# Kernel optimization log

Measured on AMD Instinct MI355X. Metric: run time of the kernel, lower is better.

Reference implementation:

```python
import jax, jax.numpy as jnp
import numpy as np

TEMPERATURE = 0.07
EPS = 1e-8  # torch CosineSimilarity eps default


def setup_inputs() -> dict:
    key = jax.random.key(0)
    k1, k2 = jax.random.split(key)
    N, D = 8192, 1024
    image_features = jax.random.normal(k1, (N, D), dtype=jnp.float32)
    text_features = jax.random.normal(k2, (N, D), dtype=jnp.float32)
    return {"image_features": image_features, "text_features": text_features}


def _normalize(x):
    # matches torch cosine similarity denominator clamp: norm >= eps
    n = jnp.sqrt(jnp.sum(x * x, axis=-1, keepdims=True))
    return x / jnp.maximum(n, EPS)


def reference(image_features, text_features):
    # cosine similarity via normalize + GEMM (same math as broadcasted NxNxD form)
    img_n = _normalize(image_features)  # [N, D]
    txt_n = _normalize(text_features)   # [N, D]
    logits = jnp.einsum('id,jd->ij', img_n, txt_n) / TEMPERATURE  # [N, N]

    N = logits.shape[0]
    labels = jnp.arange(N)
    # cross-entropy with labels = diagonal indices
    logp_i2t = jax.nn.log_softmax(logits, axis=-1)      # rows: image -> text
    logp_t2i = jax.nn.log_softmax(logits.T, axis=-1)    # rows: text -> image
    loss_i2t = -jnp.mean(logp_i2t[labels, labels])
    loss_t2i = -jnp.mean(logp_t2i[labels, labels])
    return (loss_i2t + loss_t2i) / 2
```

## Files before the change

kernel.cpp:

```cpp
#include <hip/hip_runtime.h>


#define BM 128
#define BN 128
#define BKB 128

typedef float floatx4 __attribute__((ext_vector_type(4)));
typedef int   intx4   __attribute__((ext_vector_type(4)));
typedef int   intx8   __attribute__((ext_vector_type(8)));

__device__ __forceinline__ void gload_lds16(const unsigned char* g, unsigned char* lds) {
    __builtin_amdgcn_global_load_lds(
        (const __attribute__((address_space(1))) void*)g,
        (__attribute__((address_space(3))) void*)lds,
        16, 0, 0);
}

__global__ __launch_bounds__(256)
void normalize_fp8(const float* __restrict__ img, const float* __restrict__ txt,
                   unsigned int* __restrict__ oimg, unsigned int* __restrict__ otxt,
                   float* __restrict__ sums, float* __restrict__ out, int N) {
    const int gi = blockIdx.x * 256 + threadIdx.x;
    if (gi < 2 * N) sums[gi] = 0.f;
    if (gi == 0) out[0] = 0.f;

    const int gw = blockIdx.x * 4 + (threadIdx.x >> 6);
    const int lane = threadIdx.x & 63;
    const float* in = (gw < N) ? img : txt;
    unsigned int* o = (gw < N) ? oimg : otxt;
    const int row = (gw < N) ? gw : gw - N;
    const float4* rp = (const float4*)(in + (size_t)row * 1024);

    float4 v[4];
    float ss = 0.f;
    #pragma unroll
    for (int j = 0; j < 4; ++j) {
        v[j] = rp[j * 64 + lane];
        ss += v[j].x * v[j].x + v[j].y * v[j].y + v[j].z * v[j].z + v[j].w * v[j].w;
    }
    #pragma unroll
    for (int o2 = 1; o2 < 64; o2 <<= 1) ss += __shfl_xor(ss, o2);
    const float inv = 16.0f / fmaxf(sqrtf(ss), 1e-8f);
    #pragma unroll
    for (int j = 0; j < 4; ++j) {
        int p = __builtin_amdgcn_cvt_pk_fp8_f32(v[j].x * inv, v[j].y * inv, 0, false);
        p = __builtin_amdgcn_cvt_pk_fp8_f32(v[j].z * inv, v[j].w * inv, p, true);
        o[(size_t)row * 256 + j * 64 + lane] = (unsigned int)p;
    }
}

__global__ __launch_bounds__(256)
void gemm_exp_kernel(const unsigned char* __restrict__ A,
                     const unsigned char* __restrict__ B,
                     float* __restrict__ rowsum, float* __restrict__ colsum,
                     float* __restrict__ diag, int K, float scale) {
    __shared__ unsigned char As[2 * BM * 64];
    __shared__ unsigned char Bs[2 * BN * 64];

    const int bm = blockIdx.x, bn = blockIdx.y;
    const int tid = threadIdx.x;
    const int lane = tid & 63;
    const int wave = tid >> 6;
    const int quad = lane >> 4;
    const int lanelo = lane & 15;
    const int wrow = (wave >> 1) * 64;
    const int wcol = (wave & 1) * 64;

    floatx4 acc[4][4] = {};

    const int c0 = wave * 128 + lane;
    const int c1 = c0 + 64;
    const int r0 = c0 >> 2, r1 = c1 >> 2;
    const int kg0 = ((c0 & 3) ^ ((r0 >> 1) & 3)) * 16;
    const int kg1 = ((c1 & 3) ^ ((r1 >> 1) & 3)) * 16;

    const unsigned char* pa0 = A + (size_t)bm * BM * K + (size_t)r0 * K + kg0;
    const unsigned char* pa1 = A + (size_t)bm * BM * K + (size_t)r1 * K + kg1;
    const unsigned char* pb0 = B + (size_t)bn * BN * K + (size_t)r0 * K + kg0;
    const unsigned char* pb1 = B + (size_t)bn * BN * K + (size_t)r1 * K + kg1;
    unsigned char* dA0 = As + c0 * 16;
    unsigned char* dA1 = As + c1 * 16;
    unsigned char* dB0 = Bs + c0 * 16;
    unsigned char* dB1 = Bs + c1 * 16;

    int aoff[4], boff[4];
    #pragma unroll
    for (int t = 0; t < 4; ++t) {
        const int Ra = wrow + t * 16 + lanelo;
        const int Rb = wcol + t * 16 + lanelo;
        const int cA = (quad & 1) * 2;
        aoff[t] = (quad >> 1) * 8192 + Ra * 64 + ((cA ^ ((Ra >> 1) & 3)) * 16);
        boff[t] = (quad >> 1) * 8192 + Rb * 64 + ((cA ^ ((Rb >> 1) & 3)) * 16);
    }

    for (int k0 = 0; k0 < K; k0 += BKB) {
        #pragma unroll
        for (int w = 0; w < 2; ++w) {
            gload_lds16(pa0 + w * 64, dA0 + w * 8192);
            gload_lds16(pa1 + w * 64, dA1 + w * 8192);
            gload_lds16(pb0 + w * 64, dB0 + w * 8192);
            gload_lds16(pb1 + w * 64, dB1 + w * 8192);
        }
        pa0 += BKB; pa1 += BKB; pb0 += BKB; pb1 += BKB;
        __syncthreads();

        intx8 af[4], bg[4];
        #pragma unroll
        for (int t = 0; t < 4; ++t) {
            const intx4 alo = *(const intx4*)(As + aoff[t]);
            const intx4 ahi = *(const intx4*)(As + (aoff[t] ^ 16));
            af[t] = __builtin_shufflevector(alo, ahi, 0, 1, 2, 3, 4, 5, 6, 7);
            const intx4 blo = *(const intx4*)(Bs + boff[t]);
            const intx4 bhi = *(const intx4*)(Bs + (boff[t] ^ 16));
            bg[t] = __builtin_shufflevector(blo, bhi, 0, 1, 2, 3, 4, 5, 6, 7);
        }

        #pragma unroll
        for (int tm = 0; tm < 4; ++tm)
            #pragma unroll
            for (int tn = 0; tn < 4; ++tn)
                acc[tm][tn] = __builtin_amdgcn_mfma_scale_f32_16x16x128_f8f6f4(
                    af[tm], bg[tn], acc[tm][tn],
                    0, 0,
                    0, 127,
                    0, 127);
        __syncthreads();
    }

    const int growb = bm * BM + wrow;
    const int gcolb = bn * BN + wcol;

    #pragma unroll
    for (int tm = 0; tm < 4; ++tm)
        #pragma unroll
        for (int tn = 0; tn < 4; ++tn)
            #pragma unroll
            for (int r = 0; r < 4; ++r) {
                const float l = acc[tm][tn][r] * scale;
                const int grow = growb + tm * 16 + quad * 4 + r;
                const int gcol = gcolb + tn * 16 + lanelo;
                if (grow == gcol) diag[grow] = l;
                acc[tm][tn][r] = __expf(l);
            }

    #pragma unroll
    for (int tm = 0; tm < 4; ++tm) {
        floatx4 rs = acc[tm][0] + acc[tm][1] + acc[tm][2] + acc[tm][3];
        #pragma unroll
        for (int r = 0; r < 4; ++r) {
            float v = rs[r];
            v += __shfl_xor(v, 1);
            v += __shfl_xor(v, 2);
            v += __shfl_xor(v, 4);
            v += __shfl_xor(v, 8);
            if (lanelo == 0)
                atomicAdd(&rowsum[growb + tm * 16 + quad * 4 + r], v);
        }
    }

    #pragma unroll
    for (int tn = 0; tn < 4; ++tn) {
        float cs = 0.f;
        #pragma unroll
        for (int tm = 0; tm < 4; ++tm)
            cs += acc[tm][tn][0] + acc[tm][tn][1] + acc[tm][tn][2] + acc[tm][tn][3];
        cs += __shfl_xor(cs, 16);
        cs += __shfl_xor(cs, 32);
        if (quad == 0)
            atomicAdd(&colsum[gcolb + tn * 16 + lanelo], cs);
    }
}

__global__ __launch_bounds__(256)
void final_reduce(const float* __restrict__ rowsum, const float* __restrict__ colsum,
                  const float* __restrict__ diag, float* __restrict__ out, int n) {
    const int i = blockIdx.x * 256 + threadIdx.x;
    const int t = threadIdx.x;
    float v = 0.5f * (logf(rowsum[i]) + logf(colsum[i])) - diag[i];
    #pragma unroll
    for (int o = 1; o < 64; o <<= 1) v += __shfl_xor(v, o);
    __shared__ float ws[4];
    if ((t & 63) == 0) ws[t >> 6] = v;
    __syncthreads();
    if (t == 0) atomicAdd(out, (ws[0] + ws[1] + ws[2] + ws[3]) / (float)n);
}

extern "C" void kernel_launch(void* const* d_in, const int* in_sizes, int n_in,
                              void* d_out, int out_size, void* d_ws, size_t ws_size,
                              hipStream_t stream) {
    const float* img = (const float*)d_in[0];
    const float* txt = (const float*)d_in[1];
    float* out = (float*)d_out;

    const int D = 1024;
    const int N = in_sizes[0] / D;

    unsigned char* imgq = (unsigned char*)d_ws;
    unsigned char* txtq = imgq + (size_t)N * D;
    float* rowsum = (float*)(txtq + (size_t)N * D);
    float* colsum = rowsum + N;
    float* diag = colsum + N;

    normalize_fp8<<<2 * N / 4, 256, 0, stream>>>(img, txt, (unsigned int*)imgq,
                                                 (unsigned int*)txtq, rowsum, out, N);

    dim3 grid(N / BM, N / BN);
    gemm_exp_kernel<<<grid, 256, 0, stream>>>(imgq, txtq, rowsum, colsum, diag,
                                              D, 1.0f / (256.0f * 0.07f));
    final_reduce<<<N / 256, 256, 0, stream>>>(rowsum, colsum, diag, out, N);
}
```

Measured before the change: 196.4 us.

## Load GEMM fragments directly from global memory instead of staging through LDS

The FP8 GEMM no longer stages A/B tiles in shared memory. Each lane now reads its MFMA operand fragments straight from global memory with 16-byte vector loads, which removes both block barriers and the LDS round trip. The cost is lost data sharing inside the block: each wave pair re-reads the same rows, so global and L2 traffic goes up. There is also no explicit prefetch, so load latency is hidden only by occupancy and compiler scheduling.

Result: slower. 327.3 us (+66.7%).

```diff
diff --git a/kernel.cpp b/kernel.cpp
--- a/kernel.cpp
+++ b/kernel.cpp
@@ -8,13 +8,6 @@
 typedef float floatx4 __attribute__((ext_vector_type(4)));
 typedef int   intx4   __attribute__((ext_vector_type(4)));
 typedef int   intx8   __attribute__((ext_vector_type(8)));
-
-__device__ __forceinline__ void gload_lds16(const unsigned char* g, unsigned char* lds) {
-    __builtin_amdgcn_global_load_lds(
-        (const __attribute__((address_space(1))) void*)g,
-        (__attribute__((address_space(3))) void*)lds,
-        16, 0, 0);
-}
 
 __global__ __launch_bounds__(256)
 void normalize_fp8(const float* __restrict__ img, const float* __restrict__ txt,
@@ -54,9 +47,6 @@
                      const unsigned char* __restrict__ B,
                      float* __restrict__ rowsum, float* __restrict__ colsum,
                      float* __restrict__ diag, int K, float scale) {
-    __shared__ unsigned char As[2 * BM * 64];
-    __shared__ unsigned char Bs[2 * BN * 64];
-
     const int bm = blockIdx.x, bn = blockIdx.y;
     const int tid = threadIdx.x;
     const int lane = tid & 63;
@@ -68,51 +58,30 @@
 
     floatx4 acc[4][4] = {};
 
-    const int c0 = wave * 128 + lane;
-    const int c1 = c0 + 64;
-    const int r0 = c0 >> 2, r1 = c1 >> 2;
-    const int kg0 = ((c0 & 3) ^ ((r0 >> 1) & 3)) * 16;
-    const int kg1 = ((c1 & 3) ^ ((r1 >> 1) & 3)) * 16;
-
-    const unsigned char* pa0 = A + (size_t)bm * BM * K + (size_t)r0 * K + kg0;
-    const unsigned char* pa1 = A + (size_t)bm * BM * K + (size_t)r1 * K + kg1;
-    const unsigned char* pb0 = B + (size_t)bn * BN * K + (size_t)r0 * K + kg0;
-    const unsigned char* pb1 = B + (size_t)bn * BN * K + (size_t)r1 * K + kg1;
-    unsigned char* dA0 = As + c0 * 16;
-    unsigned char* dA1 = As + c1 * 16;
-    unsigned char* dB0 = Bs + c0 * 16;
-    unsigned char* dB1 = Bs + c1 * 16;
-
-    int aoff[4], boff[4];
+    const unsigned char* pa[4];
+    const unsigned char* pb[4];
     #pragma unroll
     for (int t = 0; t < 4; ++t) {
-        const int Ra = wrow + t * 16 + lanelo;
-        const int Rb = wcol + t * 16 + lanelo;
-        const int cA = (quad & 1) * 2;
-        aoff[t] = (quad >> 1) * 8192 + Ra * 64 + ((cA ^ ((Ra >> 1) & 3)) * 16);
-        boff[t] = (quad >> 1) * 8192 + Rb * 64 + ((cA ^ ((Rb >> 1) & 3)) * 16);
+        pa[t] = A + (size_t)(bm * BM + wrow + t * 16 + lanelo) * K + quad * 32;
+        pb[t] = B + (size_t)(bn * BN + wcol + t * 16 + lanelo) * K + quad * 32;
     }
 
     for (int k0 = 0; k0 < K; k0 += BKB) {
+        intx4 a0[4], a1[4], b0[4], b1[4];
         #pragma unroll
-        for (int w = 0; w < 2; ++w) {
-            gload_lds16(pa0 + w * 64, dA0 + w * 8192);
-            gload_lds16(pa1 + w * 64, dA1 + w * 8192);
-            gload_lds16(pb0 + w * 64, dB0 + w * 8192);
-            gload_lds16(pb1 + w * 64, dB1 + w * 8192);
+        for (int t = 0; t < 4; ++t) {
+            a0[t] = *(const intx4*)(pa[t]);
+            a1[t] = *(const intx4*)(pa[t] + 16);
+            b0[t] = *(const intx4*)(pb[t]);
+            b1[t] = *(const intx4*)(pb[t] + 16);
+            pa[t] += BKB; pb[t] += BKB;
         }
-        pa0 += BKB; pa1 += BKB; pb0 += BKB; pb1 += BKB;
-        __syncthreads();
 
         intx8 af[4], bg[4];
         #pragma unroll
         for (int t = 0; t < 4; ++t) {
-            const intx4 alo = *(const intx4*)(As + aoff[t]);
-            const intx4 ahi = *(const intx4*)(As + (aoff[t] ^ 16));
-            af[t] = __builtin_shufflevector(alo, ahi, 0, 1, 2, 3, 4, 5, 6, 7);
-            const intx4 blo = *(const intx4*)(Bs + boff[t]);
-            const intx4 bhi = *(const intx4*)(Bs + (boff[t] ^ 16));
-            bg[t] = __builtin_shufflevector(blo, bhi, 0, 1, 2, 3, 4, 5, 6, 7);
+            af[t] = __builtin_shufflevector(a0[t], a1[t], 0, 1, 2, 3, 4, 5, 6, 7);
+            bg[t] = __builtin_shufflevector(b0[t], b1[t], 0, 1, 2, 3, 4, 5, 6, 7);
         }
 
         #pragma unroll
@@ -124,7 +93,6 @@
                     0, 0,
                     0, 127,
                     0, 127);
-        __syncthreads();
     }
 
     const int growb = bm * BM + wrow;
```

## Switch FP8 GEMM to 32x32x64 scaled MFMA tiles

Applied to the files above, without the earlier changes.

Replaces the 4x4 grid of 16x16x128 scaled FP8 MFMAs per wave with a 2x2 grid of 32x32x64 MFMAs, issued over two K sub-steps per 128-wide LDS tile. The LDS fragment offsets, the epilogue row/column index mapping, and the row/column sum shuffle reductions are rewritten for the 32x32 accumulator layout. The goal is fewer LDS fragment reads per MFMA and fewer instructions for the same FLOPs. It also adds a launch-bounds occupancy hint of 4 blocks, which may constrain register allocation.

Result: slower. 208.7 us (+6.3%).

```diff
diff --git a/kernel.cpp b/kernel.cpp
--- a/kernel.cpp
+++ b/kernel.cpp
@@ -5,9 +5,9 @@
 #define BN 128
 #define BKB 128
 
-typedef float floatx4 __attribute__((ext_vector_type(4)));
-typedef int   intx4   __attribute__((ext_vector_type(4)));
-typedef int   intx8   __attribute__((ext_vector_type(8)));
+typedef float floatx16 __attribute__((ext_vector_type(16)));
+typedef int   intx4    __attribute__((ext_vector_type(4)));
+typedef int   intx8    __attribute__((ext_vector_type(8)));
 
 __device__ __forceinline__ void gload_lds16(const unsigned char* g, unsigned char* lds) {
     __builtin_amdgcn_global_load_lds(
@@ -49,7 +49,7 @@
     }
 }
 
-__global__ __launch_bounds__(256)
+__global__ __launch_bounds__(256, 4)
 void gemm_exp_kernel(const unsigned char* __restrict__ A,
                      const unsigned char* __restrict__ B,
                      float* __restrict__ rowsum, float* __restrict__ colsum,
@@ -61,12 +61,12 @@
     const int tid = threadIdx.x;
     const int lane = tid & 63;
     const int wave = tid >> 6;
-    const int quad = lane >> 4;
-    const int lanelo = lane & 15;
+    const int half = lane >> 5;
+    const int l31 = lane & 31;
     const int wrow = (wave >> 1) * 64;
     const int wcol = (wave & 1) * 64;
 
-    floatx4 acc[4][4] = {};
+    floatx16 acc[2][2] = {};
 
     const int c0 = wave * 128 + lane;
     const int c1 = c0 + 64;
@@ -83,14 +83,14 @@
     unsigned char* dB0 = Bs + c0 * 16;
     unsigned char* dB1 = Bs + c1 * 16;
 
-    int aoff[4], boff[4];
-    #pragma unroll
-    for (int t = 0; t < 4; ++t) {
-        const int Ra = wrow + t * 16 + lanelo;
-        const int Rb = wcol + t * 16 + lanelo;
-        const int cA = (quad & 1) * 2;
-        aoff[t] = (quad >> 1) * 8192 + Ra * 64 + ((cA ^ ((Ra >> 1) & 3)) * 16);
-        boff[t] = (quad >> 1) * 8192 + Rb * 64 + ((cA ^ ((Rb >> 1) & 3)) * 16);
+    int aoff[2], boff[2];
+    #pragma unroll
+    for (int t = 0; t < 2; ++t) {
+        const int Ra = wrow + t * 32 + l31;
+        const int Rb = wcol + t * 32 + l31;
+        const int cf = half * 2;
+        aoff[t] = Ra * 64 + ((cf ^ ((Ra >> 1) & 3)) * 16);
+        boff[t] = Rb * 64 + ((cf ^ ((Rb >> 1) & 3)) * 16);
     }
 
     for (int k0 = 0; k0 < K; k0 += BKB) {
@@ -104,26 +104,29 @@
         pa0 += BKB; pa1 += BKB; pb0 += BKB; pb1 += BKB;
         __syncthreads();
 
-        intx8 af[4], bg[4];
-        #pragma unroll
-        for (int t = 0; t < 4; ++t) {
-            const intx4 alo = *(const intx4*)(As + aoff[t]);
-            const intx4 ahi = *(const intx4*)(As + (aoff[t] ^ 16));
-            af[t] = __builtin_shufflevector(alo, ahi, 0, 1, 2, 3, 4, 5, 6, 7);
-            const intx4 blo = *(const intx4*)(Bs + boff[t]);
-            const intx4 bhi = *(const intx4*)(Bs + (boff[t] ^ 16));
-            bg[t] = __builtin_shufflevector(blo, bhi, 0, 1, 2, 3, 4, 5, 6, 7);
+        #pragma unroll
+        for (int s = 0; s < 2; ++s) {
+            const int wofs = s * 8192;
+            intx8 af[2], bg[2];
+            #pragma unroll
+            for (int t = 0; t < 2; ++t) {
+                const intx4 alo = *(const intx4*)(As + wofs + aoff[t]);
+                const intx4 ahi = *(const intx4*)(As + wofs + (aoff[t] ^ 16));
+                af[t] = __builtin_shufflevector(alo, ahi, 0, 1, 2, 3, 4, 5, 6, 7);
+                const intx4 blo = *(const intx4*)(Bs + wofs + boff[t]);
+                const intx4 bhi = *(const intx4*)(Bs + wofs + (boff[t] ^ 16));
+                bg[t] = __builtin_shufflevector(blo, bhi, 0, 1, 2, 3, 4, 5, 6, 7);
+            }
+            #pragma unroll
+            for (int tm = 0; tm < 2; ++tm)
+                #pragma unroll
+                for (int tn = 0; tn < 2; ++tn)
+                    acc[tm][tn] = __builtin_amdgcn_mfma_scale_f32_32x32x64_f8f6f4(
+                        af[tm], bg[tn], acc[tm][tn],
+                        0, 0,
+                        0, 127,
+                        0, 127);
         }
-
-        #pragma unroll
-        for (int tm = 0; tm < 4; ++tm)
-            #pragma unroll
-            for (int tn = 0; tn < 4; ++tn)
-                acc[tm][tn] = __builtin_amdgcn_mfma_scale_f32_16x16x128_f8f6f4(
-                    af[tm], bg[tn], acc[tm][tn],
-                    0, 0,
-                    0, 127,
-                    0, 127);
         __syncthreads();
     }
 
@@ -131,43 +134,44 @@
     const int gcolb = bn * BN + wcol;
 
     #pragma unroll
-    for (int tm = 0; tm < 4; ++tm)
-        #pragma unroll
-        for (int tn = 0; tn < 4; ++tn)
-            #pragma unroll
-            for (int r = 0; r < 4; ++r) {
+    for (int tm = 0; tm < 2; ++tm)
+        #pragma unroll
+        for (int tn = 0; tn < 2; ++tn)
+            #pragma unroll
+            for (int r = 0; r < 16; ++r) {
                 const float l = acc[tm][tn][r] * scale;
-                const int grow = growb + tm * 16 + quad * 4 + r;
-                const int gcol = gcolb + tn * 16 + lanelo;
+                const int grow = growb + tm * 32 + (r & 3) + 8 * (r >> 2) + 4 * half;
+                const int gcol = gcolb + tn * 32 + l31;
                 if (grow == gcol) diag[grow] = l;
                 acc[tm][tn][r] = __expf(l);
             }
 
     #pragma unroll
-    for (int tm = 0; tm < 4; ++tm) {
-        floatx4 rs = acc[tm][0] + acc[tm][1] + acc[tm][2] + acc[tm][3];
-        #pragma unroll
-        for (int r = 0; r < 4; ++r) {
-            float v = rs[r];
+    for (int tm = 0; tm < 2; ++tm) {
+        #pragma unroll
+        for (int r = 0; r < 16; ++r) {
+            float v = acc[tm][0][r] + acc[tm][1][r];
             v += __shfl_xor(v, 1);
             v += __shfl_xor(v, 2);
             v += __shfl_xor(v, 4);
             v += __shfl_xor(v, 8);
-            if (lanelo == 0)
-                atomicAdd(&rowsum[growb + tm * 16 + quad * 4 + r], v);
+            v += __shfl_xor(v, 16);
+            if (l31 == 0)
+                atomicAdd(&rowsum[growb + tm * 32 + (r & 3) + 8 * (r >> 2) + 4 * half], v);
         }
     }
 
     #pragma unroll
-    for (int tn = 0; tn < 4; ++tn) {
+    for (int tn = 0; tn < 2; ++tn) {
         float cs = 0.f;
         #pragma unroll
-        for (int tm = 0; tm < 4; ++tm)
-            cs += acc[tm][tn][0] + acc[tm][tn][1] + acc[tm][tn][2] + acc[tm][tn][3];
-        cs += __shfl_xor(cs, 16);
+        for (int tm = 0; tm < 2; ++tm)
+            #pragma unroll
+            for (int r = 0; r < 16; ++r)
+                cs += acc[tm][tn][r];
         cs += __shfl_xor(cs, 32);
-        if (quad == 0)
-            atomicAdd(&colsum[gcolb + tn * 16 + lanelo], cs);
+        if (half == 0)
+            atomicAdd(&colsum[gcolb + tn * 32 + l31], cs);
     }
 }
 
```
